# Kernel optimization log

Hardware: AMD Instinct MI355X
Metric: run time of the kernel (lower is better)

The kernel has to match this reference:

```python
import jax, jax.numpy as jnp
import numpy as np

B, V, N, S, F, H, K, STEPS = 8, 3, 400, 1200, 16, 32, 10, 12
ALPHA_FUSE = 0.8
NEG = -9e15


def setup_inputs() -> dict:
    key = jax.random.key(0)
    ks = jax.random.split(key, 16)
    g = lambda i, shape, s=0.1: jax.random.normal(ks[i], shape, jnp.float32) * s
    return {
        "feat": jax.random.normal(ks[0], (B, S, F), jnp.float32),
        "adj": jax.random.bernoulli(ks[1], 0.05, (B, V, S, S)).astype(jnp.float32),
        "dis_lab": jax.random.uniform(ks[2], (B, K), dtype=jnp.float32),
        "W_gat": g(3, (V, F, H), 0.3),
        "a_gat": g(4, (V, 2 * H, 1), 0.3),
        "qkv_W": g(5, (H, 3 * H)),
        "qkv_b": jnp.zeros((3 * H,), jnp.float32),
        "o_W": g(6, (H, H)),
        "o_b": jnp.zeros((H,), jnp.float32),
        "fus_W": g(7, (H, H)),
        "fus_b": jnp.zeros((H,), jnp.float32),
        "att1_W": g(8, (2 * H, H)),
        "att1_b": jnp.zeros((H,), jnp.float32),
        "att2_W": g(9, (H, 1)),
        "att2_b": jnp.zeros((1,), jnp.float32),
        "gru_Wih": g(10, (H, 3 * H)),
        "gru_Whh": g(11, (H, 3 * H)),
        "gru_bih": jnp.zeros((3 * H,), jnp.float32),
        "gru_bhh": jnp.zeros((3 * H,), jnp.float32),
        "out_W": g(12, (H, 1)),
        "out_b": jnp.zeros((1,), jnp.float32),
    }


def _forward(feat, adj, dis_lab, W_gat, a_gat, qkv_W, qkv_b, o_W, o_b,
             fus_W, fus_b, att1_W, att1_b, att2_W, att2_b,
             gru_Wih, gru_Whh, gru_bih, gru_bhh, out_W, out_b):
    # ---- per-view GAT (masked softmax over dense adjacency) ----
    Wh = jnp.einsum('bsf,vfh->bvsh', feat, W_gat)            # [B,V,S,H]
    a1, a2 = a_gat[:, :H, 0], a_gat[:, H:, 0]
    e = (jnp.einsum('bvsh,vh->bvs', Wh, a1)[..., :, None]
         + jnp.einsum('bvsh,vh->bvs', Wh, a2)[..., None, :])  # [B,V,S,S]
    e = jax.nn.leaky_relu(e, 0.2)
    e = jnp.where(adj > 0, e, NEG)
    att = jax.nn.softmax(e, axis=-1)
    hid = jax.nn.elu(jnp.einsum('bvst,bvth->bvsh', att, Wh))  # [B,V,S,H]
    # ---- cross-view self-attention fusion (single head) ----
    x = hid.reshape(B, V * S, H)
    q, k, v = jnp.split(x @ qkv_W + qkv_b, 3, axis=-1)
    logits = jnp.einsum('bld,bmd->blm', q, k) / jnp.sqrt(jnp.float32(H))
    sa = jnp.einsum('blm,bmd->bld', jax.nn.softmax(logits, axis=-1), v)
    sa = sa @ o_W + o_b
    hfuse = (ALPHA_FUSE * sa + (1.0 - ALPHA_FUSE) * x).reshape(B, V, S, H)
    gate = jax.nn.sigmoid(hfuse @ fus_W + fus_b)
    fusion = jnp.sum(gate * hfuse, axis=1)[:, 2 * N:, :]      # [B,N,H]
    # ---- attention over label stations ----
    label = fusion[:, :K, :]                                  # [B,K,H]
    unlabel = fusion[:, K, :]                                 # [B,H]
    cat = jnp.concatenate([label, jnp.broadcast_to(unlabel[:, None, :], label.shape)], axis=-1)
    s = jax.nn.relu(cat @ att1_W + att1_b) @ att2_W + att2_b  # [B,K,1]
    score = jax.nn.softmax(s[..., 0] * dis_lab, axis=1)
    ctx = jnp.einsum('bk,bkh->bh', score, label)
    # ---- GRU decoder (feed hidden state back as next input) ----
    def gru_cell(xt, h):
        gi = xt @ gru_Wih + gru_bih
        gh = h @ gru_Whh + gru_bhh
        ir, iz, inn = jnp.split(gi, 3, axis=-1)
        hr, hz, hn = jnp.split(gh, 3, axis=-1)
        r = jax.nn.sigmoid(ir + hr)
        z = jax.nn.sigmoid(iz + hz)
        n = jnp.tanh(inn + r * hn)
        return (1.0 - z) * n + z * h
    def step(carry, _):
        xt, h = carry
        h2 = gru_cell(xt, h)
        out = h2 @ out_W + out_b
        return (h2, h2), out[:, 0]
    _, outs = jax.lax.scan(step, (ctx, unlabel), None, length=STEPS)
    return outs.T  # [B, STEPS]


def reference(feat, adj, dis_lab, W_gat, a_gat, qkv_W, qkv_b, o_W, o_b,
              fus_W, fus_b, att1_W, att1_b, att2_W, att2_b,
              gru_Wih, gru_Whh, gru_bih, gru_bhh, out_W, out_b):
    return _forward(feat, adj, dis_lab, W_gat, a_gat, qkv_W, qkv_b, o_W, o_b,
                    fus_W, fus_b, att1_W, att1_b, att2_W, att2_b,
                    gru_Wih, gru_Whh, gru_bih, gru_bhh, out_W, out_b)
```

## Files before the change

kernel.cpp:

```cpp
#include <hip/hip_runtime.h>
#include <math.h>

#define Bb 8
#define Vv 3
#define Ss 1200
#define SgP 1280
#define Ff 16
#define Hh 32
#define Kk 10
#define STEPS 12
#define ROWS (Bb*Vv*Ss)
#define L (Vv*Ss)
#define KPAD 1280
#define NKB 160
#define MROW 40

typedef __attribute__((ext_vector_type(8))) short bf16x8;
typedef __attribute__((ext_vector_type(4))) float f32x4;
typedef __attribute__((ext_vector_type(4))) unsigned int u32x4;

__device__ __forceinline__ unsigned int pack_hi2(float x0, float x1) {
    return (__float_as_uint(x1) & 0xFFFF0000u) | (__float_as_uint(x0) >> 16);
}
__device__ __forceinline__ unsigned int pack_lo2(float x0, float x1) {
    float h0 = __uint_as_float(__float_as_uint(x0) & 0xFFFF0000u);
    float h1 = __uint_as_float(__float_as_uint(x1) & 0xFFFF0000u);
    return (__float_as_uint(x1 - h1) & 0xFFFF0000u) | (__float_as_uint(x0 - h0) >> 16);
}
__device__ __forceinline__ unsigned int spread4(unsigned int x) {
    x = (x | (x << 12)) & 0x000F000Fu;
    x = (x | (x << 6))  & 0x03030303u;
    x = (x | (x << 3))  & 0x11111111u;
    return x;
}

__global__ __launch_bounds__(256) void gat_wh_k(const float* __restrict__ feat,
                                                const float* __restrict__ W_gat,
                                                const float* __restrict__ a_gat,
                                                float* __restrict__ Wh,
                                                float* __restrict__ fvec,
                                                float* __restrict__ gvecP) {
    int blk = blockIdx.x;
    int c = blk % 150;
    int v = (blk / 150) % Vv;
    int b = blk / (150 * Vv);
    int tid = threadIdx.x;
    int r = tid >> 5;
    int h = tid & 31;
    int s = c * 8 + r;

    __shared__ float Wg[16][32];
    __shared__ float fe[8][16];
    for (int i = tid; i < 512; i += 256) Wg[i >> 5][i & 31] = W_gat[v * 512 + i];
    for (int i = tid; i < 128; i += 256) fe[i >> 4][i & 15] = feat[(b * Ss + c * 8) * Ff + i];
    __syncthreads();

    float acc = 0.f;
#pragma unroll
    for (int k = 0; k < 16; ++k) acc += fe[r][k] * Wg[k][h];

    int bv = b * Vv + v;
    int row = bv * Ss + s;
    Wh[(size_t)row * Hh + h] = acc;

    float a1 = a_gat[v * 64 + h];
    float a2 = a_gat[v * 64 + 32 + h];
    float pf = acc * a1, pg = acc * a2;
#pragma unroll
    for (int m = 16; m >= 1; m >>= 1) {
        pf += __shfl_xor(pf, m);
        pg += __shfl_xor(pg, m);
    }
    if (h == 0) { fvec[row] = pf; gvecP[(size_t)bv * SgP + s] = pg; }
}

__global__ __launch_bounds__(256) void gmax_k(float* __restrict__ gvecP,
                                              float* __restrict__ Gmax) {
    int bv = blockIdx.x;
    int tid = threadIdx.x;
    if (tid < SgP - Ss) gvecP[(size_t)bv * SgP + Ss + tid] = 0.f;
    float m = -3.0e38f;
    for (int t = tid; t < Ss; t += 256) m = fmaxf(m, gvecP[(size_t)bv * SgP + t]);
#pragma unroll
    for (int mm = 32; mm >= 1; mm >>= 1) m = fmaxf(m, __shfl_xor(m, mm));
    __shared__ float red[4];
    if ((tid & 63) == 0) red[tid >> 6] = m;
    __syncthreads();
    if (tid == 0) Gmax[bv] = fmaxf(fmaxf(red[0], red[1]), fmaxf(red[2], red[3]));
}

__global__ __launch_bounds__(256) void wht_k(const float* __restrict__ Wh,
                                             ushort* __restrict__ WhT) {
    int bv = blockIdx.x / 20, t = blockIdx.x % 20;
    int s0 = t * 64;
    int tid = threadIdx.x;
    __shared__ float T[64][33];
    for (int idx = tid; idx < 2048; idx += 256) {
        int r = idx >> 5, h = idx & 31;
        T[r][h] = (s0 + r < Ss) ? Wh[((size_t)bv * Ss + s0 + r) * Hh + h] : 0.f;
    }
    __syncthreads();
    int h = tid >> 3, c = tid & 7;
    int kb = t * 8 + c;
    unsigned int hb[4], lb[4];
#pragma unroll
    for (int j = 0; j < 4; ++j) {
        float e0 = T[c * 8 + 2 * j][h], e1 = T[c * 8 + 2 * j + 1][h];
        hb[j] = pack_hi2(e0, e1);
        lb[j] = pack_lo2(e0, e1);
    }
    size_t base = (((size_t)bv * NKB + kb) * 2) * 256 + h * 8;
    *(uint4*)(WhT + base)       = make_uint4(hb[0], hb[1], hb[2], hb[3]);
    *(uint4*)(WhT + base + 256) = make_uint4(lb[0], lb[1], lb[2], lb[3]);
}

__global__ __launch_bounds__(256) void adj_pack_k(const float* __restrict__ adj,
                                                  unsigned int* __restrict__ maskb) {
    int gw = (blockIdx.x * 256 + threadIdx.x) >> 6;
    int lane = threadIdx.x & 63;
    for (int row = gw; row < ROWS; row += 5760) {
        const float* ar = adj + (size_t)row * Ss;
        unsigned int* mrow = maskb + (size_t)row * MROW;
#pragma unroll
        for (int c = 0; c < 5; ++c) {
            int base = c * 256 + lane * 4;
            bool v = (base + 3) < Ss;
            float4 a = v ? *(const float4*)(ar + base) : make_float4(0.f, 0.f, 0.f, 0.f);
            unsigned long long b0 = __ballot(v && (a.x > 0.f));
            unsigned long long b1 = __ballot(v && (a.y > 0.f));
            unsigned long long b2 = __ballot(v && (a.z > 0.f));
            unsigned long long b3 = __ballot(v && (a.w > 0.f));
            int nw = (c == 4) ? 6 : 8;
            if (lane < nw) {
                int sh = 8 * lane;
                unsigned int B0 = (unsigned int)(b0 >> sh) & 0xFFu;
                unsigned int B1 = (unsigned int)(b1 >> sh) & 0xFFu;
                unsigned int B2 = (unsigned int)(b2 >> sh) & 0xFFu;
                unsigned int B3 = (unsigned int)(b3 >> sh) & 0xFFu;
                mrow[c * 8 + lane] = spread4(B0) | (spread4(B1) << 1)
                                   | (spread4(B2) << 2) | (spread4(B3) << 3);
            }
        }
        if (lane < 2) mrow[38 + lane] = 0u;
    }
}

__global__ __launch_bounds__(256) void gat_mfma_k(const unsigned int* __restrict__ maskb,
                                                  const ushort* __restrict__ WhT,
                                                  const float* __restrict__ fvec,
                                                  const float* __restrict__ gvecP,
                                                  const float* __restrict__ Gmax,
                                                  float* __restrict__ hid,
                                                  float* __restrict__ hsel) {
    int blk = blockIdx.x;
    int bv = blk / 75, tb = blk % 75;
    int wk = threadIdx.x >> 6, lane = threadIdx.x & 63;
    int rowbase = tb * 16;
    int lr = lane & 15, kg = lane >> 4;
    int b = bv / Vv, v = bv - b * Vv;

    int ar = rowbase + lr;
    const float* g_b = gvecP + (size_t)bv * SgP;
    float fr = fvec[bv * Ss + ar];
    float M = fr + Gmax[bv];
    float Mr = fmaxf(M, 0.2f * M);

    const unsigned int* mrow = maskb + (size_t)(bv * Ss + ar) * MROW + wk * 10;
    unsigned int mw[10];
#pragma unroll
    for (int i = 0; i < 5; ++i) {
        uint2 t = *(const uint2*)(mrow + 2 * i);
        mw[2 * i] = t.x; mw[2 * i + 1] = t.y;
    }

    f32x4 acc0 = {0.f, 0.f, 0.f, 0.f}, acc1 = {0.f, 0.f, 0.f, 0.f};
    float psum = 0.f;
    const ushort* Wbv = WhT + ((size_t)bv * NKB) * 512;

    int kst = wk * 320;
#pragma unroll
    for (int s = 0; s < 10; ++s) {
        int t0 = kst + s * 32 + kg * 8;
        int kb = t0 >> 3;
        unsigned int mb = (mw[s] >> (kg * 8)) & 0xFFu;

        const ushort* Bp = Wbv + (size_t)kb * 512 + lr * 8;
        bf16x8 bh0 = *(const bf16x8*)(Bp);
        bf16x8 bh1 = *(const bf16x8*)(Bp + 128);
        bf16x8 bl0 = *(const bf16x8*)(Bp + 256);
        bf16x8 bl1 = *(const bf16x8*)(Bp + 384);

        float4 gA = *(const float4*)(g_b + t0);
        float4 gB = *(const float4*)(g_b + t0 + 4);
        float gv8[8] = {gA.x, gA.y, gA.z, gA.w, gB.x, gB.y, gB.z, gB.w};
        float p[8];
#pragma unroll
        for (int j = 0; j < 8; ++j) {
            float e = fr + gv8[j];
            e = fmaxf(e, 0.2f * e);
            float pe = __expf(e - Mr);
            p[j] = ((mb >> j) & 1u) ? pe : 0.f;
            psum += p[j];
        }
        unsigned int hbp[4], lbp[4];
#pragma unroll
        for (int j = 0; j < 4; ++j) {
            hbp[j] = pack_hi2(p[2 * j], p[2 * j + 1]);
            lbp[j] = pack_lo2(p[2 * j], p[2 * j + 1]);
        }
        bf16x8 ah = __builtin_bit_cast(bf16x8, (u32x4){hbp[0], hbp[1], hbp[2], hbp[3]});
        bf16x8 al = __builtin_bit_cast(bf16x8, (u32x4){lbp[0], lbp[1], lbp[2], lbp[3]});
        acc0 = __builtin_amdgcn_mfma_f32_16x16x32_bf16(ah, bh0, acc0, 0, 0, 0);
        acc0 = __builtin_amdgcn_mfma_f32_16x16x32_bf16(ah, bl0, acc0, 0, 0, 0);
        acc0 = __builtin_amdgcn_mfma_f32_16x16x32_bf16(al, bh0, acc0, 0, 0, 0);
        acc1 = __builtin_amdgcn_mfma_f32_16x16x32_bf16(ah, bh1, acc1, 0, 0, 0);
        acc1 = __builtin_amdgcn_mfma_f32_16x16x32_bf16(ah, bl1, acc1, 0, 0, 0);
        acc1 = __builtin_amdgcn_mfma_f32_16x16x32_bf16(al, bh1, acc1, 0, 0, 0);
    }

    psum += __shfl_xor(psum, 16);
    psum += __shfl_xor(psum, 32);

    __shared__ float accS[4][2][16][17];
    __shared__ float psS[4][16];
#pragma unroll
    for (int j = 0; j < 4; ++j) {
        accS[wk][0][kg * 4 + j][lr] = acc0[j];
        accS[wk][1][kg * 4 + j][lr] = acc1[j];
    }
    if (lane < 16) psS[wk][lr] = psum;
    __syncthreads();
    if (threadIdx.x < 16)
        psS[0][threadIdx.x] += psS[1][threadIdx.x] + psS[2][threadIdx.x] + psS[3][threadIdx.x];
    __syncthreads();

    bool qb = (tb == 50);
    for (int idx = threadIdx.x; idx < 512; idx += 256) {
        int r = idx >> 5, col = idx & 31, tt = col >> 4, c = col & 15;
        float a = accS[0][tt][r][c] + accS[1][tt][r][c] + accS[2][tt][r][c] + accS[3][tt][r][c];
        float rr = a / psS[0][r];
        float hv = (rr > 0.f) ? rr : expm1f(rr);
        hid[((size_t)bv * Ss + rowbase + r) * 32 + col] = hv;
        if (qb && r < 11) hsel[(((size_t)b * Vv + v) * 11 + r) * 32 + col] = hv;
    }
}

__global__ __launch_bounds__(256) void attn_q_k(const float* __restrict__ hsel,
                                                const float* __restrict__ qkv_W,
                                                const float* __restrict__ qkv_b,
                                                float* __restrict__ qt,
                                                float* __restrict__ qc) {
    int b = blockIdx.x;
    int tid = threadIdx.x;
    __shared__ float hq[33][33];
    __shared__ float W1[32][33];
    __shared__ float W2[32][33];
    __shared__ float qS[33][33];

    for (int idx = tid; idx < 33 * 32; idx += 256) {
        int q = idx >> 5, i = idx & 31;
        int si = q / 3, v = q - si * 3;
        hq[q][i] = hsel[(((size_t)b * Vv + v) * 11 + si) * 32 + i];
    }
    for (int idx = tid; idx < 1024; idx += 256) {
        int i = idx >> 5, j = idx & 31;
        W1[i][j] = qkv_W[i * 96 + j];
        W2[i][j] = qkv_W[i * 96 + 32 + j];
    }
    __syncthreads();
    for (int idx = tid; idx < 33 * 32; idx += 256) {
        int q = idx >> 5, j = idx & 31;
        float a = qkv_b[j];
#pragma unroll
        for (int i = 0; i < 32; ++i) a += hq[q][i] * W1[i][j];
        qS[q][j] = a;
    }
    __syncthreads();
    for (int idx = tid; idx < 33 * 32; idx += 256) {
        int q = idx >> 5, i = idx & 31;
        float a = 0.f;
#pragma unroll
        for (int j = 0; j < 32; ++j) a += qS[q][j] * W2[i][j];
        qt[(size_t)b * 33 * 32 + q * 32 + i] = a;
    }
    if (tid < 33) {
        float a = 0.f;
        for (int j = 0; j < 32; ++j) a += qS[tid][j] * qkv_b[32 + j];
        qc[b * 33 + tid] = a;
    }
}

#define CH 120
#define NCH 30
#define PREC 34
__global__ __launch_bounds__(256) void attn_part_k(const float* __restrict__ hid,
                                                   const float* __restrict__ qt,
                                                   const float* __restrict__ qc,
                                                   float* __restrict__ part) {
    int blk = blockIdx.x;
    int b = blk / NCH, ch = blk % NCH;
    int k0 = ch * CH;
    int tid = threadIdx.x;
    const float inv = 0.1767766952966369f;

    __shared__ float hC[CH][33];
    __shared__ float qtS[33][33];
    __shared__ float qcS[33];
    __shared__ float lS[33][124];
    __shared__ float mS[33], lsS[33];

    for (int idx = tid; idx < CH * 32; idx += 256) {
        int r = idx >> 5, i = idx & 31;
        hC[r][i] = hid[((size_t)b * L + k0 + r) * 32 + i];
    }
    for (int idx = tid; idx < 33 * 32; idx += 256) {
        int q = idx >> 5, i = idx & 31;
        qtS[q][i] = qt[(size_t)b * 33 * 32 + q * 32 + i];
    }
    if (tid < 33) qcS[tid] = qc[b * 33 + tid];
    __syncthreads();

    for (int idx = tid; idx < 33 * CH; idx += 256) {
        int q = idx / CH, m = idx - q * CH;
        float d = 0.f;
#pragma unroll
        for (int i = 0; i < 32; ++i) d += qtS[q][i] * hC[m][i];
        lS[q][m] = (d + qcS[q]) * inv;
    }
    __syncthreads();

    int q4 = tid >> 2, j4 = tid & 3;
    if (q4 < 33) {
        float m = -3.0e38f;
        for (int k = j4; k < CH; k += 4) m = fmaxf(m, lS[q4][k]);
        m = fmaxf(m, __shfl_xor(m, 1));
        m = fmaxf(m, __shfl_xor(m, 2));
        float ssum = 0.f;
        for (int k = j4; k < CH; k += 4) {
            float p = __expf(lS[q4][k] - m);
            lS[q4][k] = p;
            ssum += p;
        }
        ssum += __shfl_xor(ssum, 1);
        ssum += __shfl_xor(ssum, 2);
        if (j4 == 0) { mS[q4] = m; lsS[q4] = ssum; }
    }
    __syncthreads();

    float* po = part + ((size_t)b * NCH + ch) * (33 * PREC);
    for (int idx = tid; idx < 33 * 32; idx += 256) {
        int q = idx >> 5, hh = idx & 31;
        float a = 0.f;
        for (int k = 0; k < CH; k += 4) {
            float4 p4 = *(const float4*)&lS[q][k];
            a += p4.x * hC[k][hh] + p4.y * hC[k+1][hh] + p4.z * hC[k+2][hh] + p4.w * hC[k+3][hh];
        }
        po[q * PREC + hh] = a;
    }
    if (tid < 33) { po[tid * PREC + 32] = mS[tid]; po[tid * PREC + 33] = lsS[tid]; }
}

__global__ __launch_bounds__(256) void attn_comb_k(const float* __restrict__ part,
                                                   const float* __restrict__ hsel,
                                                   const float* __restrict__ qkv_W,
                                                   const float* __restrict__ qkv_b,
                                                   const float* __restrict__ o_W,
                                                   const float* __restrict__ o_b,
                                                   const float* __restrict__ fus_W,
                                                   const float* __restrict__ fus_b,
                                                   float* __restrict__ hfg) {
    int b = blockIdx.x;
    int tid = threadIdx.x;
    __shared__ float RS[33][NCH];
    __shared__ float LSs[33];
    __shared__ float oS[33][33];
    __shared__ float vS[33][33];
    __shared__ float hfS[33][33];
    const float* pb = part + (size_t)b * NCH * (33 * PREC);

    if (tid < 33) {
        float M = -3.0e38f;
        for (int c = 0; c < NCH; ++c) M = fmaxf(M, pb[c * 33 * PREC + tid * PREC + 32]);
        float Lt = 0.f;
        for (int c = 0; c < NCH; ++c) {
            float w = __expf(pb[c * 33 * PREC + tid * PREC + 32] - M);
            RS[tid][c] = w;
            Lt += w * pb[c * 33 * PREC + tid * PREC + 33];
        }
        LSs[tid] = Lt;
    }
    __syncthreads();

    for (int idx = tid; idx < 33 * 32; idx += 256) {
        int q = idx >> 5, hh = idx & 31;
        float a = 0.f;
        for (int c = 0; c < NCH; ++c) a += RS[q][c] * pb[c * 33 * PREC + q * PREC + hh];
        oS[q][hh] = a / LSs[q];
    }
    __syncthreads();
    for (int idx = tid; idx < 33 * 32; idx += 256) {
        int q = idx >> 5, j = idx & 31;
        float a = qkv_b[64 + j];
#pragma unroll
        for (int i = 0; i < 32; ++i) a += oS[q][i] * qkv_W[i * 96 + 64 + j];
        vS[q][j] = a;
    }
    __syncthreads();
    for (int idx = tid; idx < 33 * 32; idx += 256) {
        int q = idx >> 5, hh = idx & 31;
        int si = q / 3, v = q - si * 3;
        float o = o_b[hh];
#pragma unroll
        for (int i = 0; i < 32; ++i) o += vS[q][i] * o_W[i * 32 + hh];
        float x = hsel[(((size_t)b * Vv + v) * 11 + si) * Hh + hh];
        hfS[q][hh] = 0.8f * o + 0.2f * x;
    }
    __syncthreads();
    for (int idx = tid; idx < 33 * 32; idx += 256) {
        int q = idx >> 5, hh = idx & 31;
        float gacc = fus_b[hh];
#pragma unroll
        for (int i = 0; i < 32; ++i) gacc += hfS[q][i] * fus_W[i * 32 + hh];
        float gate = 1.f / (1.f + __expf(-gacc));
        hfg[(size_t)(b * 33 + q) * 32 + hh] = gate * hfS[q][hh];
    }
}

__global__ __launch_bounds__(64) void head_k(const float* __restrict__ hfg,
                                             const float* __restrict__ dis_lab,
                                             const float* __restrict__ att1_W,
                                             const float* __restrict__ att1_b,
                                             const float* __restrict__ att2_W,
                                             const float* __restrict__ att2_b,
                                             const float* __restrict__ Wih,
                                             const float* __restrict__ Whh,
                                             const float* __restrict__ bih,
                                             const float* __restrict__ bhh,
                                             const float* __restrict__ out_W,
                                             const float* __restrict__ out_b,
                                             float* __restrict__ out) {
    int b = blockIdx.x;
    int tid = threadIdx.x;
    int j = tid & 31, half = tid >> 5;

    __shared__ float lab[11][32];
    __shared__ float a1T[32][68];
    __shared__ float WihT[3][32][36];
    __shared__ float WhhT[3][32][36];
    __shared__ float sc[12];
    __shared__ float xS[32], hS[32];

    for (int i = tid; i < 352; i += 64) {
        int k = i >> 5, hh = i & 31;
        float val = 0.f;
#pragma unroll
        for (int v = 0; v < 3; ++v) val += hfg[(size_t)(b * 33 + k * 3 + v) * 32 + hh];
        lab[k][hh] = val;
    }
    for (int idx = tid; idx < 2048; idx += 64) {
        int i = idx >> 5, jj = idx & 31;
        a1T[jj][i] = att1_W[idx];
    }
    for (int idx = tid; idx < 3072; idx += 64) {
        int i = idx / 96, col = idx - i * 96;
        int g = col >> 5, jj = col & 31;
        WihT[g][jj][i] = Wih[idx];
        WhhT[g][jj][i] = Whh[idx];
    }
    __syncthreads();

    float a2w = att2_W[j];
    float a1b = att1_b[j];
    float a2b = att2_b[0];
#pragma unroll
    for (int kk = 0; kk < 5; ++kk) {
        int k = 2 * kk + half;
        float t1 = a1b;
#pragma unroll
        for (int c = 0; c < 8; ++c) {
            float4 lb4 = *(const float4*)&lab[k][c * 4];
            float4 w4  = *(const float4*)&a1T[j][c * 4];
            t1 += lb4.x * w4.x + lb4.y * w4.y + lb4.z * w4.z + lb4.w * w4.w;
        }
#pragma unroll
        for (int c = 0; c < 8; ++c) {
            float4 lb4 = *(const float4*)&lab[10][c * 4];
            float4 w4  = *(const float4*)&a1T[j][32 + c * 4];
            t1 += lb4.x * w4.x + lb4.y * w4.y + lb4.z * w4.z + lb4.w * w4.w;
        }
        float val = fmaxf(t1, 0.f) * a2w;
#pragma unroll
        for (int mm = 16; mm >= 1; mm >>= 1) val += __shfl_xor(val, mm);
        if (j == 0) sc[k] = (val + a2b) * dis_lab[b * Kk + k];
    }
    __syncthreads();
    if (tid == 0) {
        float mx = sc[0];
        for (int k = 1; k < 10; ++k) mx = fmaxf(mx, sc[k]);
        float sm = 0.f;
        for (int k = 0; k < 10; ++k) { sc[k] = __expf(sc[k] - mx); sm += sc[k]; }
        for (int k = 0; k < 10; ++k) sc[k] /= sm;
    }
    __syncthreads();
    if (tid < 32) {
        float c = 0.f;
        for (int k = 0; k < 10; ++k) c += sc[k] * lab[k][tid];
        xS[tid] = c;
        hS[tid] = lab[10][tid];
    }
    __syncthreads();

    float b_ir = bih[j], b_iz = bih[32 + j], b_in = bih[64 + j];
    float b_hr = bhh[j], b_hz = bhh[32 + j], b_hn = bhh[64 + j];
    float ow = out_W[j], ob = out_b[0];
    int i0 = half * 16;

    for (int t = 0; t < STEPS; ++t) {
        float gi_r = 0.f, gi_z = 0.f, gi_n = 0.f;
        float gh_r = 0.f, gh_z = 0.f, gh_n = 0.f;
#pragma unroll
        for (int c = 0; c < 4; ++c) {
            float4 x4 = *(const float4*)&xS[i0 + c * 4];
            float4 h4 = *(const float4*)&hS[i0 + c * 4];
            float4 wr = *(const float4*)&WihT[0][j][i0 + c * 4];
            float4 wz = *(const float4*)&WihT[1][j][i0 + c * 4];
            float4 wn = *(const float4*)&WihT[2][j][i0 + c * 4];
            float4 ur = *(const float4*)&WhhT[0][j][i0 + c * 4];
            float4 uz = *(const float4*)&WhhT[1][j][i0 + c * 4];
            float4 un = *(const float4*)&WhhT[2][j][i0 + c * 4];
            gi_r += x4.x * wr.x + x4.y * wr.y + x4.z * wr.z + x4.w * wr.w;
            gi_z += x4.x * wz.x + x4.y * wz.y + x4.z * wz.z + x4.w * wz.w;
            gi_n += x4.x * wn.x + x4.y * wn.y + x4.z * wn.z + x4.w * wn.w;
            gh_r += h4.x * ur.x + h4.y * ur.y + h4.z * ur.z + h4.w * ur.w;
            gh_z += h4.x * uz.x + h4.y * uz.y + h4.z * uz.z + h4.w * uz.w;
            gh_n += h4.x * un.x + h4.y * un.y + h4.z * un.z + h4.w * un.w;
        }
        gi_r += __shfl_xor(gi_r, 32); gi_z += __shfl_xor(gi_z, 32); gi_n += __shfl_xor(gi_n, 32);
        gh_r += __shfl_xor(gh_r, 32); gh_z += __shfl_xor(gh_z, 32); gh_n += __shfl_xor(gh_n, 32);

        float hprev = hS[j];
        float r = 1.f / (1.f + __expf(-(gi_r + b_ir + gh_r + b_hr)));
        float z = 1.f / (1.f + __expf(-(gi_z + b_iz + gh_z + b_hz)));
        float n = tanhf(gi_n + b_in + r * (gh_n + b_hn));
        float hnew = (1.f - z) * n + z * hprev;

        float outp = hnew * ow;
#pragma unroll
        for (int mm = 16; mm >= 1; mm >>= 1) outp += __shfl_xor(outp, mm);
        if (tid == 0) out[b * STEPS + t] = outp + ob;
        __syncthreads();
        if (tid < 32) { hS[tid] = hnew; xS[tid] = hnew; }
        __syncthreads();
    }
}

extern "C" void kernel_launch(void* const* d_in, const int* in_sizes, int n_in,
                              void* d_out, int out_size, void* d_ws, size_t ws_size,
                              hipStream_t stream) {
    const float* feat    = (const float*)d_in[0];
    const float* adj     = (const float*)d_in[1];
    const float* dis_lab = (const float*)d_in[2];
    const float* W_gat   = (const float*)d_in[3];
    const float* a_gat   = (const float*)d_in[4];
    const float* qkv_W   = (const float*)d_in[5];
    const float* qkv_b   = (const float*)d_in[6];
    const float* o_W     = (const float*)d_in[7];
    const float* o_b     = (const float*)d_in[8];
    const float* fus_W   = (const float*)d_in[9];
    const float* fus_b   = (const float*)d_in[10];
    const float* att1_W  = (const float*)d_in[11];
    const float* att1_b  = (const float*)d_in[12];
    const float* att2_W  = (const float*)d_in[13];
    const float* att2_b  = (const float*)d_in[14];
    const float* Wih     = (const float*)d_in[15];
    const float* Whh     = (const float*)d_in[16];
    const float* bih     = (const float*)d_in[17];
    const float* bhh     = (const float*)d_in[18];
    const float* out_W   = (const float*)d_in[19];
    const float* out_b   = (const float*)d_in[20];
    float* out = (float*)d_out;

    float* ws = (float*)d_ws;
    float*  Wh     = ws;
    float*  hid    = ws;
    float*  fvec   = ws + 921600;
    float*  gvecP  = ws + 950400;
    float*  Gmax   = ws + 981120;
    ushort* WhT    = (ushort*)(ws + 981152);
    float*  part   = ws + 981152;
    float*  hsel   = ws + 1964192;
    float*  hfg    = ws + 1972640;
    float*  qt     = ws + 1981088;
    float*  qc     = ws + 1989536;
    unsigned int* maskb = (unsigned int*)(ws + 1989824);

    adj_pack_k<<<dim3(1440), dim3(256), 0, stream>>>(adj, maskb);
    gat_wh_k<<<dim3(Bb * Vv * 150), dim3(256), 0, stream>>>(feat, W_gat, a_gat, Wh, fvec, gvecP);
    gmax_k<<<dim3(Bb * Vv), dim3(256), 0, stream>>>(gvecP, Gmax);
    wht_k<<<dim3(Bb * Vv * 20), dim3(256), 0, stream>>>(Wh, WhT);
    gat_mfma_k<<<dim3(Bb * Vv * 75), dim3(256), 0, stream>>>(maskb, WhT,
                                                             fvec, gvecP, Gmax, hid, hsel);
    attn_q_k<<<dim3(Bb), dim3(256), 0, stream>>>(hsel, qkv_W, qkv_b, qt, qc);
    attn_part_k<<<dim3(Bb * NCH), dim3(256), 0, stream>>>(hid, qt, qc, part);
    attn_comb_k<<<dim3(Bb), dim3(256), 0, stream>>>(part, hsel, qkv_W, qkv_b,
                                                    o_W, o_b, fus_W, fus_b, hfg);
    head_k<<<dim3(Bb), dim3(64), 0, stream>>>(hfg, dis_lab, att1_W, att1_b, att2_W, att2_b,
                                              Wih, Whh, bih, bhh, out_W, out_b, out);
}
```

Before: 131.3 us.

## Fuse Wh projection with bf16 transpose-pack; batch adj loads; add occupancy hint

Merges the Wh projection kernel and the split-bf16 transpose/pack kernel into one kernel, so the fp32 Wh intermediate is never written to or re-read from global memory and one launch is removed. The fused kernel computes 64 rows per block in eight passes into shared memory, then packs them. The adjacency packing loop now issues all five float4 loads before any ballots, to increase memory-level parallelism. gat_mfma_k gets a min-blocks-per-CU launch bound of 4, which may limit registers per thread.

```diff
diff --git a/kernel.cpp b/kernel.cpp
--- a/kernel.cpp
+++ b/kernel.cpp
@@ -34,44 +34,63 @@
     return x;
 }
 
-__global__ __launch_bounds__(256) void gat_wh_k(const float* __restrict__ feat,
+__global__ __launch_bounds__(256) void wh_wht_k(const float* __restrict__ feat,
                                                 const float* __restrict__ W_gat,
                                                 const float* __restrict__ a_gat,
-                                                float* __restrict__ Wh,
+                                                ushort* __restrict__ WhT,
                                                 float* __restrict__ fvec,
                                                 float* __restrict__ gvecP) {
-    int blk = blockIdx.x;
-    int c = blk % 150;
-    int v = (blk / 150) % Vv;
-    int b = blk / (150 * Vv);
+    int bv = blockIdx.x / 20, t = blockIdx.x % 20;
+    int b = bv / Vv, v = bv - b * Vv;
+    int s0 = t * 64;
     int tid = threadIdx.x;
-    int r = tid >> 5;
-    int h = tid & 31;
-    int s = c * 8 + r;
-
+
+    __shared__ float T[64][33];
     __shared__ float Wg[16][32];
-    __shared__ float fe[8][16];
     for (int i = tid; i < 512; i += 256) Wg[i >> 5][i & 31] = W_gat[v * 512 + i];
-    for (int i = tid; i < 128; i += 256) fe[i >> 4][i & 15] = feat[(b * Ss + c * 8) * Ff + i];
-    __syncthreads();
-
-    float acc = 0.f;
-#pragma unroll
-    for (int k = 0; k < 16; ++k) acc += fe[r][k] * Wg[k][h];
-
-    int bv = b * Vv + v;
-    int row = bv * Ss + s;
-    Wh[(size_t)row * Hh + h] = acc;
-
+    __syncthreads();
+
+    int r8 = tid >> 5, h = tid & 31;
     float a1 = a_gat[v * 64 + h];
     float a2 = a_gat[v * 64 + 32 + h];
-    float pf = acc * a1, pg = acc * a2;
-#pragma unroll
-    for (int m = 16; m >= 1; m >>= 1) {
-        pf += __shfl_xor(pf, m);
-        pg += __shfl_xor(pg, m);
-    }
-    if (h == 0) { fvec[row] = pf; gvecP[(size_t)bv * SgP + s] = pg; }
+#pragma unroll
+    for (int pass = 0; pass < 8; ++pass) {
+        int s = s0 + pass * 8 + r8;
+        float acc = 0.f;
+        if (s < Ss) {
+            const float4* fe = (const float4*)(feat + ((size_t)b * Ss + s) * Ff);
+            float4 f0 = fe[0], f1 = fe[1], f2 = fe[2], f3 = fe[3];
+            acc += f0.x * Wg[0][h]  + f0.y * Wg[1][h]  + f0.z * Wg[2][h]  + f0.w * Wg[3][h];
+            acc += f1.x * Wg[4][h]  + f1.y * Wg[5][h]  + f1.z * Wg[6][h]  + f1.w * Wg[7][h];
+            acc += f2.x * Wg[8][h]  + f2.y * Wg[9][h]  + f2.z * Wg[10][h] + f2.w * Wg[11][h];
+            acc += f3.x * Wg[12][h] + f3.y * Wg[13][h] + f3.z * Wg[14][h] + f3.w * Wg[15][h];
+        }
+        T[pass * 8 + r8][h] = acc;
+        float pf = acc * a1, pg = acc * a2;
+#pragma unroll
+        for (int m = 16; m >= 1; m >>= 1) {
+            pf += __shfl_xor(pf, m);
+            pg += __shfl_xor(pg, m);
+        }
+        if (h == 0 && s < Ss) {
+            fvec[bv * Ss + s] = pf;
+            gvecP[(size_t)bv * SgP + s] = pg;
+        }
+    }
+    __syncthreads();
+
+    int hh = tid >> 3, c = tid & 7;
+    int kb = t * 8 + c;
+    unsigned int hb[4], lb[4];
+#pragma unroll
+    for (int j = 0; j < 4; ++j) {
+        float e0 = T[c * 8 + 2 * j][hh], e1 = T[c * 8 + 2 * j + 1][hh];
+        hb[j] = pack_hi2(e0, e1);
+        lb[j] = pack_lo2(e0, e1);
+    }
+    size_t base = (((size_t)bv * NKB + kb) * 2) * 256 + hh * 8;
+    *(uint4*)(WhT + base)       = make_uint4(hb[0], hb[1], hb[2], hb[3]);
+    *(uint4*)(WhT + base + 256) = make_uint4(lb[0], lb[1], lb[2], lb[3]);
 }
 
 __global__ __launch_bounds__(256) void gmax_k(float* __restrict__ gvecP,
@@ -89,31 +108,6 @@
     if (tid == 0) Gmax[bv] = fmaxf(fmaxf(red[0], red[1]), fmaxf(red[2], red[3]));
 }
 
-__global__ __launch_bounds__(256) void wht_k(const float* __restrict__ Wh,
-                                             ushort* __restrict__ WhT) {
-    int bv = blockIdx.x / 20, t = blockIdx.x % 20;
-    int s0 = t * 64;
-    int tid = threadIdx.x;
-    __shared__ float T[64][33];
-    for (int idx = tid; idx < 2048; idx += 256) {
-        int r = idx >> 5, h = idx & 31;
-        T[r][h] = (s0 + r < Ss) ? Wh[((size_t)bv * Ss + s0 + r) * Hh + h] : 0.f;
-    }
-    __syncthreads();
-    int h = tid >> 3, c = tid & 7;
-    int kb = t * 8 + c;
-    unsigned int hb[4], lb[4];
-#pragma unroll
-    for (int j = 0; j < 4; ++j) {
-        float e0 = T[c * 8 + 2 * j][h], e1 = T[c * 8 + 2 * j + 1][h];
-        hb[j] = pack_hi2(e0, e1);
-        lb[j] = pack_lo2(e0, e1);
-    }
-    size_t base = (((size_t)bv * NKB + kb) * 2) * 256 + h * 8;
-    *(uint4*)(WhT + base)       = make_uint4(hb[0], hb[1], hb[2], hb[3]);
-    *(uint4*)(WhT + base + 256) = make_uint4(lb[0], lb[1], lb[2], lb[3]);
-}
-
 __global__ __launch_bounds__(256) void adj_pack_k(const float* __restrict__ adj,
                                                   unsigned int* __restrict__ maskb) {
     int gw = (blockIdx.x * 256 + threadIdx.x) >> 6;
@@ -121,15 +115,19 @@
     for (int row = gw; row < ROWS; row += 5760) {
         const float* ar = adj + (size_t)row * Ss;
         unsigned int* mrow = maskb + (size_t)row * MROW;
+        float4 a[5];
 #pragma unroll
         for (int c = 0; c < 5; ++c) {
             int base = c * 256 + lane * 4;
-            bool v = (base + 3) < Ss;
-            float4 a = v ? *(const float4*)(ar + base) : make_float4(0.f, 0.f, 0.f, 0.f);
-            unsigned long long b0 = __ballot(v && (a.x > 0.f));
-            unsigned long long b1 = __ballot(v && (a.y > 0.f));
-            unsigned long long b2 = __ballot(v && (a.z > 0.f));
-            unsigned long long b3 = __ballot(v && (a.w > 0.f));
+            a[c] = (base + 3 < Ss) ? *(const float4*)(ar + base)
+                                   : make_float4(0.f, 0.f, 0.f, 0.f);
+        }
+#pragma unroll
+        for (int c = 0; c < 5; ++c) {
+            unsigned long long b0 = __ballot(a[c].x > 0.f);
+            unsigned long long b1 = __ballot(a[c].y > 0.f);
+            unsigned long long b2 = __ballot(a[c].z > 0.f);
+            unsigned long long b3 = __ballot(a[c].w > 0.f);
             int nw = (c == 4) ? 6 : 8;
             if (lane < nw) {
                 int sh = 8 * lane;
@@ -145,13 +143,13 @@
     }
 }
 
-__global__ __launch_bounds__(256) void gat_mfma_k(const unsigned int* __restrict__ maskb,
-                                                  const ushort* __restrict__ WhT,
-                                                  const float* __restrict__ fvec,
-                                                  const float* __restrict__ gvecP,
-                                                  const float* __restrict__ Gmax,
-                                                  float* __restrict__ hid,
-                                                  float* __restrict__ hsel) {
+__global__ __launch_bounds__(256, 4) void gat_mfma_k(const unsigned int* __restrict__ maskb,
+                                                     const ushort* __restrict__ WhT,
+                                                     const float* __restrict__ fvec,
+                                                     const float* __restrict__ gvecP,
+                                                     const float* __restrict__ Gmax,
+                                                     float* __restrict__ hid,
+                                                     float* __restrict__ hsel) {
     int blk = blockIdx.x;
     int bv = blk / 75, tb = blk % 75;
     int wk = threadIdx.x >> 6, lane = threadIdx.x & 63;
@@ -581,7 +579,6 @@
     float* out = (float*)d_out;
 
     float* ws = (float*)d_ws;
-    float*  Wh     = ws;
     float*  hid    = ws;
     float*  fvec   = ws + 921600;
     float*  gvecP  = ws + 950400;
@@ -595,9 +592,9 @@
     unsigned int* maskb = (unsigned int*)(ws + 1989824);
 
     adj_pack_k<<<dim3(1440), dim3(256), 0, stream>>>(adj, maskb);
-    gat_wh_k<<<dim3(Bb * Vv * 150), dim3(256), 0, stream>>>(feat, W_gat, a_gat, Wh, fvec, gvecP);
+    wh_wht_k<<<dim3(Bb * Vv * 20), dim3(256), 0, stream>>>(feat, W_gat, a_gat,
+                                                           WhT, fvec, gvecP);
     gmax_k<<<dim3(Bb * Vv), dim3(256), 0, stream>>>(gvecP, Gmax);
-    wht_k<<<dim3(Bb * Vv * 20), dim3(256), 0, stream>>>(Wh, WhT);
     gat_mfma_k<<<dim3(Bb * Vv * 75), dim3(256), 0, stream>>>(maskb, WhT,
                                                              fvec, gvecP, Gmax, hid, hsel);
     attn_q_k<<<dim3(Bb), dim3(256), 0, stream>>>(hsel, qkv_W, qkv_b, qt, qc);
```

New measurement: 130.0 us. No clear change (-1.0%).
